# Kernel tuning notes

Measured on AMD Instinct MI355X. Metric: run time of the kernel, lower is better.

Reference implementation:

```python
import jax, jax.numpy as jnp
import numpy as np

EPS = 1e-12  # tf.nn.l2_normalize epsilon used by keras Dot(normalize=True)

def setup_inputs() -> dict:
    key = jax.random.key(0)
    k1, k2 = jax.random.split(key)
    a = jax.random.normal(k1, (16, 4096, 256), dtype=jnp.float32)
    b = jax.random.normal(k2, (16, 4096, 256), dtype=jnp.float32)
    return {"a": a, "b": b}

def _l2_normalize(x, axis=-1):
    # matches tf.nn.l2_normalize: x * rsqrt(max(sum(x^2), eps))
    sq = jnp.sum(x * x, axis=axis, keepdims=True)
    return x * jax.lax.rsqrt(jnp.maximum(sq, EPS))

def reference(a, b):
    # Original: full [B,N,N] cosine-similarity matrix then diag_part.
    # The diagonal equals the rowwise cosine similarity, computed directly.
    an = _l2_normalize(a, axis=2)  # [B, N, D]
    bn = _l2_normalize(b, axis=2)  # [B, N, D]
    return jnp.sum(an * bn, axis=2)  # [B, N]
```

## Files before the change

### kernel.cpp

```cpp
#include <hip/hip_runtime.h>


#define D 256
#define EPS 1e-12f

__global__ __launch_bounds__(256) void cosine_rows_kernel(
    const float* __restrict__ a,
    const float* __restrict__ b,
    float* __restrict__ out,
    int n_rows)
{
    const int lane = threadIdx.x & 63;
    const int wave = threadIdx.x >> 6;
    const int row  = blockIdx.x * 4 + wave;
    if (row >= n_rows) return;

    const float4* a4 = reinterpret_cast<const float4*>(a + (size_t)row * D);
    const float4* b4 = reinterpret_cast<const float4*>(b + (size_t)row * D);

    float4 av = a4[lane];
    float4 bv = b4[lane];

    float sa  = av.x * av.x + av.y * av.y + av.z * av.z + av.w * av.w;
    float sb  = bv.x * bv.x + bv.y * bv.y + bv.z * bv.z + bv.w * bv.w;
    float sab = av.x * bv.x + av.y * bv.y + av.z * bv.z + av.w * bv.w;

    #pragma unroll
    for (int off = 32; off > 0; off >>= 1) {
        sa  += __shfl_xor(sa,  off, 64);
        sb  += __shfl_xor(sb,  off, 64);
        sab += __shfl_xor(sab, off, 64);
    }

    if (lane == 0) {
        out[row] = sab * rsqrtf(fmaxf(sa, EPS)) * rsqrtf(fmaxf(sb, EPS));
    }
}

extern "C" void kernel_launch(void* const* d_in, const int* in_sizes, int n_in,
                              void* d_out, int out_size, void* d_ws, size_t ws_size,
                              hipStream_t stream)
{
    const float* a = (const float*)d_in[0];
    const float* b = (const float*)d_in[1];
    float* out = (float*)d_out;

    const int n_rows = out_size;
    const int rows_per_block = 4;
    const int grid = (n_rows + rows_per_block - 1) / rows_per_block;

    cosine_rows_kernel<<<grid, 256, 0, stream>>>(a, b, out, n_rows);
}
```

Before: 138.3 us.

## Process eight rows per wave with eight lanes per row and deeper loads

Each wave now handles eight rows, with eight lanes per row and each lane issuing eight float4 loads from a and b. This raises memory-level parallelism per thread, cuts the shuffle reduction from six steps to three, and lowers the block count eightfold. In exchange there are fewer total waves in flight, each access instruction spans eight rows, and register use per thread goes up.

```diff
diff --git a/kernel.cpp b/kernel.cpp
--- a/kernel.cpp
+++ b/kernel.cpp
@@ -1,8 +1,13 @@
 #include <hip/hip_runtime.h>
 
 
-#define D 256
-#define EPS 1e-12f
+#define D          256
+#define D4         64
+#define EPS        1e-12f
+#define LANES_ROW  8
+#define ROWS_WAVE  8
+#define F4_LANE    8
+#define WAVES_BLK  4
 
 __global__ __launch_bounds__(256) void cosine_rows_kernel(
     const float* __restrict__ a,
@@ -12,27 +17,38 @@
 {
     const int lane = threadIdx.x & 63;
     const int wave = threadIdx.x >> 6;
-    const int row  = blockIdx.x * 4 + wave;
+    const int g    = lane >> 3;
+    const int s    = lane & 7;
+
+    const int row = (blockIdx.x * WAVES_BLK + wave) * ROWS_WAVE + g;
     if (row >= n_rows) return;
 
-    const float4* a4 = reinterpret_cast<const float4*>(a + (size_t)row * D);
-    const float4* b4 = reinterpret_cast<const float4*>(b + (size_t)row * D);
+    const float4* a4 = reinterpret_cast<const float4*>(a) + (size_t)row * D4 + s;
+    const float4* b4 = reinterpret_cast<const float4*>(b) + (size_t)row * D4 + s;
 
-    float4 av = a4[lane];
-    float4 bv = b4[lane];
+    float4 av[F4_LANE], bv[F4_LANE];
+    #pragma unroll
+    for (int k = 0; k < F4_LANE; ++k) {
+        av[k] = a4[k * LANES_ROW];
+        bv[k] = b4[k * LANES_ROW];
+    }
 
-    float sa  = av.x * av.x + av.y * av.y + av.z * av.z + av.w * av.w;
-    float sb  = bv.x * bv.x + bv.y * bv.y + bv.z * bv.z + bv.w * bv.w;
-    float sab = av.x * bv.x + av.y * bv.y + av.z * bv.z + av.w * bv.w;
+    float sa = 0.f, sb = 0.f, sab = 0.f;
+    #pragma unroll
+    for (int k = 0; k < F4_LANE; ++k) {
+        sa  += av[k].x * av[k].x + av[k].y * av[k].y + av[k].z * av[k].z + av[k].w * av[k].w;
+        sb  += bv[k].x * bv[k].x + bv[k].y * bv[k].y + bv[k].z * bv[k].z + bv[k].w * bv[k].w;
+        sab += av[k].x * bv[k].x + av[k].y * bv[k].y + av[k].z * bv[k].z + av[k].w * bv[k].w;
+    }
 
     #pragma unroll
-    for (int off = 32; off > 0; off >>= 1) {
+    for (int off = 1; off < LANES_ROW; off <<= 1) {
         sa  += __shfl_xor(sa,  off, 64);
         sb  += __shfl_xor(sb,  off, 64);
         sab += __shfl_xor(sab, off, 64);
     }
 
-    if (lane == 0) {
+    if (s == 0) {
         out[row] = sab * rsqrtf(fmaxf(sa, EPS)) * rsqrtf(fmaxf(sb, EPS));
     }
 }
@@ -46,7 +62,7 @@
     float* out = (float*)d_out;
 
     const int n_rows = out_size;
-    const int rows_per_block = 4;
+    const int rows_per_block = WAVES_BLK * ROWS_WAVE;
     const int grid = (n_rows + rows_per_block - 1) / rows_per_block;
 
     cosine_rows_kernel<<<grid, 256, 0, stream>>>(a, b, out, n_rows);
```

New measurement: 142.6 us. 3.1% more time.
